# Optimization experiments

Measured on AMD Instinct MI355X. Metric: run time of the kernel, lower is better.

The kernel has to match this reference:

```python
import jax, jax.numpy as jnp
import numpy as np

B, S, D = 2, 2048, 2048
H = 32
HD = D // H  # 64
EPS = 1e-4


def setup_inputs() -> dict:
    key = jax.random.key(0)
    ks = jax.random.split(key, 9)
    hidden_states = jax.random.normal(ks[0], (B, S, D), dtype=jnp.float32)
    # multiplicative causal mask
    attention_mask = jnp.tril(jnp.ones((S, S), dtype=jnp.float32))[None, None]
    scale = 0.02
    wq = jax.random.normal(ks[1], (D, D), dtype=jnp.float32) * scale
    wk = jax.random.normal(ks[2], (D, D), dtype=jnp.float32) * scale
    wv = jax.random.normal(ks[3], (D, D), dtype=jnp.float32) * scale
    wo = jax.random.normal(ks[4], (D, D), dtype=jnp.float32) * scale
    bq = jax.random.normal(ks[5], (D,), dtype=jnp.float32) * scale
    bk = jax.random.normal(ks[6], (D,), dtype=jnp.float32) * scale
    bv = jax.random.normal(ks[7], (D,), dtype=jnp.float32) * scale
    bo = jax.random.normal(ks[8], (D,), dtype=jnp.float32) * scale
    return {"hidden_states": hidden_states, "attention_mask": attention_mask,
            "wq": wq, "bq": bq, "wk": wk, "bk": bk, "wv": wv, "bv": bv,
            "wo": wo, "bo": bo}


def _split_heads(x):
    # [B, S, D] -> [B, H, S, HD]
    b, s, _ = x.shape
    return x.reshape(b, s, H, HD).transpose(0, 2, 1, 3)


def reference(hidden_states, attention_mask, wq, bq, wk, bk, wv, bv, wo, bo):
    scaling = HD ** -0.5
    q = (hidden_states @ wq.T + bq) * scaling
    k = hidden_states @ wk.T + bk
    v = hidden_states @ wv.T + bv
    q, k, v = _split_heads(q), _split_heads(k), _split_heads(v)
    # ELU+1 feature map, then sum-normalize over head dim
    q = jax.nn.elu(q) + 1.0
    k = jax.nn.elu(k) + 1.0
    q = q / (q.sum(-1, keepdims=True) + EPS)
    k = k / (k.sum(-1, keepdims=True) + EPS)
    # quadratic attention: [B, H, S, S]
    attn = jnp.einsum('bhsd,bhtd->bhst', q, k) * (HD ** -0.5)
    attn = attn * attention_mask  # multiplicative mask
    out = jnp.einsum('bhst,bhtd->bhsd', attn, v)  # [B, H, S, HD]
    out = out.transpose(0, 2, 1, 3).reshape(hidden_states.shape[0], -1, D)
    return out @ wo.T + bo
```

## Files before the change

kernel.cpp:

```cpp
#include <hip/hip_runtime.h>

typedef __bf16 bf16x8 __attribute__((ext_vector_type(8)));
typedef float f32x4 __attribute__((ext_vector_type(4)));

#define GLDS(g, l) __builtin_amdgcn_global_load_lds(                              \
    (const __attribute__((address_space(1))) void*)(g),                            \
    (__attribute__((address_space(3))) void*)(l), 16, 0, 0)

__device__ __forceinline__ unsigned short f2bf(float f) {
  unsigned int u = __builtin_bit_cast(unsigned int, f);
  u = (u + 0x7fffu + ((u >> 16) & 1u)) >> 16;
  return (unsigned short)u;
}
__device__ __forceinline__ float bf2f(unsigned short h) {
  unsigned int u = ((unsigned int)h) << 16;
  return __builtin_bit_cast(float, u);
}

__global__ __launch_bounds__(256) void cvt_f32_bf16(
    const float* __restrict__ in, unsigned short* __restrict__ out, int n4) {
  int i = blockIdx.x * 256 + threadIdx.x;
  if (i < n4) {
    float4 v = ((const float4*)in)[i];
    ushort4 o;
    o.x = f2bf(v.x); o.y = f2bf(v.y); o.z = f2bf(v.z); o.w = f2bf(v.w);
    ((ushort4*)out)[i] = o;
  }
}

__global__ __launch_bounds__(256) void cvt_w4(
    const float* __restrict__ w0, const float* __restrict__ w1,
    const float* __restrict__ w2, const float* __restrict__ w3,
    unsigned short* __restrict__ out) {
  const int y = blockIdx.y;
  const float* src = (y == 0) ? w0 : (y == 1) ? w1 : (y == 2) ? w2 : w3;
  const int i = blockIdx.x * 256 + threadIdx.x;
  float4 v = ((const float4*)src)[i];
  ushort4 o;
  o.x = f2bf(v.x); o.y = f2bf(v.y); o.z = f2bf(v.z); o.w = f2bf(v.w);
  ((ushort4*)(out + (size_t)y * 4194304))[i] = o;
}

__global__ __launch_bounds__(512, 2) void gemm384_qkv(
    const unsigned short* __restrict__ A, const unsigned short* __restrict__ Bw,
    const float* __restrict__ bq, const float* __restrict__ bk, const float* __restrict__ bv,
    unsigned short* __restrict__ oQ, unsigned short* __restrict__ oK,
    unsigned short* __restrict__ oV) {
  constexpr int K = 2048, NT = 32;
  __shared__ unsigned short lds[81920];
  const int tid = threadIdx.x, lane = tid & 63, wid = tid >> 6;
  const int wm = wid >> 1, wn = wid & 1;

  const int g0 = blockIdx.x;
  const int wg = (g0 & 7) * 32 + (g0 >> 3);
  const int chunk = wg >> 5, l = wg & 31;
  const int bx = (chunk & 3) * 4 + (l >> 3);
  const int by = (chunk >> 2) * 8 + (l & 7);

  const int rloc = tid >> 3;
  const size_t gcoff = (size_t)(((lane & 7) ^ (lane >> 3)) << 3);
  const unsigned short* gA = A  + (size_t)(by * 256 + rloc) * K + gcoff;
  const unsigned short* gB = Bw + (size_t)(bx * 384 + rloc) * K + gcoff;

#define ABu(b) ((b) * 16384)
#define BBu(b) (32768 + (b) * 24576)
#define STAGE_A(c, b) GLDS(gA + (size_t)(c) * 64 * K, lds + ABu(b) + (c) * 4096 + wid * 512)
#define STAGE_B(c, b) GLDS(gB + (size_t)(c) * 64 * K, lds + BBu(b) + (c) * 4096 + wid * 512)

  const int arow = (wm * 64 + (lane & 15)) * 64;
  const int brow = (wn * 192 + (lane & 15)) * 64;
  const int sw0 = (((lane >> 4)) ^ (lane & 7)) << 3;
  const int sw1 = ((4 + (lane >> 4)) ^ (lane & 7)) << 3;

  f32x4 acc[4][12] = {};

  STAGE_A(0, 0); STAGE_A(1, 0); STAGE_A(2, 0); STAGE_A(3, 0);
  STAGE_B(0, 0); STAGE_B(1, 0); STAGE_B(2, 0); STAGE_B(3, 0); STAGE_B(4, 0); STAGE_B(5, 0);
  gA += 64; gB += 64;
  asm volatile("s_waitcnt vmcnt(0)" ::: "memory");
  __builtin_amdgcn_s_barrier();

  for (int t = 0; t < NT; ++t) {
    const int Ab = ABu(t & 1) + arow;
    const int Bb = BBu(t & 1) + brow;
    const int sb = (t + 1) & 1;
    const bool st = (t + 1 < NT);
    bf16x8 Af[4], Bf[6];

    if (st) { STAGE_B(0, sb); STAGE_B(1, sb); STAGE_B(2, sb); }
#pragma unroll
    for (int m = 0; m < 4; ++m) Af[m] = *(const bf16x8*)&lds[Ab + m * 1024 + sw0];
#pragma unroll
    for (int n = 0; n < 6; ++n) Bf[n] = *(const bf16x8*)&lds[Bb + n * 1024 + sw0];
    __builtin_amdgcn_s_barrier();
    __builtin_amdgcn_s_setprio(1);
#pragma unroll
    for (int m = 0; m < 4; ++m)
#pragma unroll
      for (int n = 0; n < 6; ++n)
        acc[m][n] = __builtin_amdgcn_mfma_f32_16x16x32_bf16(Af[m], Bf[n], acc[m][n], 0, 0, 0);
    __builtin_amdgcn_s_setprio(0);
    __builtin_amdgcn_s_barrier();

    if (st) { STAGE_B(3, sb); STAGE_B(4, sb); STAGE_B(5, sb); }
#pragma unroll
    for (int n = 0; n < 6; ++n) Bf[n] = *(const bf16x8*)&lds[Bb + (n + 6) * 1024 + sw0];
    __builtin_amdgcn_s_barrier();
    __builtin_amdgcn_s_setprio(1);
#pragma unroll
    for (int m = 0; m < 4; ++m)
#pragma unroll
      for (int n = 0; n < 6; ++n)
        acc[m][n + 6] = __builtin_amdgcn_mfma_f32_16x16x32_bf16(Af[m], Bf[n], acc[m][n + 6], 0, 0, 0);
    __builtin_amdgcn_s_setprio(0);
    __builtin_amdgcn_s_barrier();

    if (st) { STAGE_A(0, sb); STAGE_A(1, sb); STAGE_A(2, sb); STAGE_A(3, sb); }
#pragma unroll
    for (int m = 0; m < 4; ++m) Af[m] = *(const bf16x8*)&lds[Ab + m * 1024 + sw1];
#pragma unroll
    for (int n = 0; n < 6; ++n) Bf[n] = *(const bf16x8*)&lds[Bb + n * 1024 + sw1];
    __builtin_amdgcn_s_barrier();
    __builtin_amdgcn_s_setprio(1);
#pragma unroll
    for (int m = 0; m < 4; ++m)
#pragma unroll
      for (int n = 0; n < 6; ++n)
        acc[m][n] = __builtin_amdgcn_mfma_f32_16x16x32_bf16(Af[m], Bf[n], acc[m][n], 0, 0, 0);
    __builtin_amdgcn_s_setprio(0);
    __builtin_amdgcn_s_barrier();

#pragma unroll
    for (int n = 0; n < 6; ++n) Bf[n] = *(const bf16x8*)&lds[Bb + (n + 6) * 1024 + sw1];
    __builtin_amdgcn_s_barrier();
    __builtin_amdgcn_s_setprio(1);
#pragma unroll
    for (int m = 0; m < 4; ++m)
#pragma unroll
      for (int n = 0; n < 6; ++n)
        acc[m][n + 6] = __builtin_amdgcn_mfma_f32_16x16x32_bf16(Af[m], Bf[n], acc[m][n + 6], 0, 0, 0);
    __builtin_amdgcn_s_setprio(0);
    if (st) {
      gA += 64; gB += 64;
      asm volatile("s_waitcnt vmcnt(0)" ::: "memory");
    }
    __builtin_amdgcn_s_barrier();
  }

  const int head0 = bx * 6 + wn * 3;
#pragma unroll
  for (int g = 0; g < 3; ++g) {
    const int head = head0 + g;
    const int type = head >> 5;
    const int h = head & 31;
    const float* bias = (type == 0) ? bq : (type == 1) ? bk : bv;
    unsigned short* dst = (type == 0) ? oQ : (type == 1) ? oK : oV;
    float bv4[4];
#pragma unroll
    for (int j = 0; j < 4; ++j) bv4[j] = bias[h * 64 + j * 16 + (lane & 15)];
#pragma unroll
    for (int m = 0; m < 4; ++m) {
#pragma unroll
      for (int r = 0; r < 4; ++r) {
        const int row = by * 256 + wm * 64 + m * 16 + ((lane >> 4) << 2) + r;
        const int bb = row >> 11, s = row & 2047;
        float e[4];
        float loc = 0.f;
#pragma unroll
        for (int j = 0; j < 4; ++j) {
          float v = acc[m][g * 4 + j][r] + bv4[j];
          if (type == 0) v *= 0.125f;
          if (type < 2) v = (v > 0.f) ? (v + 1.f) : __expf(v);
          e[j] = v; loc += v;
        }
        if (type < 2) {
#pragma unroll
          for (int off = 1; off < 16; off <<= 1) loc += __shfl_xor(loc, off, 64);
          const float inv = 1.f / (loc + 1e-4f);
#pragma unroll
          for (int j = 0; j < 4; ++j) e[j] *= inv;
        }
        const size_t base = ((size_t)((bb << 5) + h) * 2048 + s) * 64;
#pragma unroll
        for (int j = 0; j < 4; ++j) dst[base + j * 16 + (lane & 15)] = f2bf(e[j]);
      }
    }
  }
#undef ABu
#undef BBu
#undef STAGE_A
#undef STAGE_B
}

__global__ __launch_bounds__(512, 2) void gemm128_wo(
    const unsigned short* __restrict__ A, const unsigned short* __restrict__ Bw,
    const float* __restrict__ b0, float* __restrict__ C) {
  constexpr int K = 2048, NT = 32;
  __shared__ unsigned short lds[73728];
  const int tid = threadIdx.x, lane = tid & 63, wid = tid >> 6;
  const int wm = wid >> 2, wn = wid & 3;

  const int g0 = blockIdx.x;
  const int wg = (g0 & 7) * 32 + (g0 >> 3);
  const int l = wg % 32;
  const int chunk = wg / 32;
  const int bx2 = (chunk % 4) * 2 + l / 16;
  const int by2 = (chunk / 4) * 16 + l % 16;

  const int rloc = wid * 8 + (lane >> 3);
  const size_t gcoff = (size_t)(((lane & 7) ^ (lane >> 3)) << 3);
  const unsigned short* gA[2];
  const unsigned short* gB[4];
#pragma unroll
  for (int c = 0; c < 2; ++c) gA[c] = A + (size_t)(by2 * 128 + c * 64 + rloc) * K + gcoff;
#pragma unroll
  for (int c = 0; c < 4; ++c) gB[c] = Bw + (size_t)(bx2 * 256 + c * 64 + rloc) * K + gcoff;

  int aoff[4][2], boff[4][2];
#pragma unroll
  for (int m = 0; m < 4; ++m)
#pragma unroll
    for (int kk = 0; kk < 2; ++kk) {
      aoff[m][kk] = (wm * 64 + m * 16 + (lane & 15)) * 64 +
                    ((((kk << 2) + (lane >> 4)) ^ (lane & 7)) << 3);
      boff[m][kk] = (wn * 64 + m * 16 + (lane & 15)) * 64 +
                    ((((kk << 2) + (lane >> 4)) ^ (lane & 7)) << 3);
    }

  f32x4 acc[4][4] = {};

#define AB(b) ((b) * 8192)
#define BB(b) (24576 + (b) * 16384)
#define STAGE_A(c, b) GLDS(gA[c], lds + AB(b) + (c) * 4096 + wid * 512)
#define STAGE_B(c, b) GLDS(gB[c], lds + BB(b) + (c) * 4096 + wid * 512)

  STAGE_A(0, 0); STAGE_A(1, 0); STAGE_B(0, 0); STAGE_B(1, 0); STAGE_B(2, 0); STAGE_B(3, 0);
#pragma unroll
  for (int c = 0; c < 2; ++c) gA[c] += 64;
#pragma unroll
  for (int c = 0; c < 4; ++c) gB[c] += 64;
  STAGE_A(0, 1); STAGE_A(1, 1); STAGE_B(0, 1); STAGE_B(1, 1); STAGE_B(2, 1); STAGE_B(3, 1);
#pragma unroll
  for (int c = 0; c < 2; ++c) gA[c] += 64;
#pragma unroll
  for (int c = 0; c < 4; ++c) gB[c] += 64;
  asm volatile("s_waitcnt vmcnt(6)" ::: "memory");
  __builtin_amdgcn_s_barrier();

  for (int t = 0; t < NT; ++t) {
    const int b = t % 3;
    const int sb = (t + 2) % 3;
    const bool doStage = (t + 2 < NT);

    if (doStage) { STAGE_A(0, sb); STAGE_A(1, sb); STAGE_B(0, sb); STAGE_B(1, sb); }
    bf16x8 af[4], bfr[4];
#pragma unroll
    for (int m = 0; m < 4; ++m) af[m] = *(const bf16x8*)&lds[AB(b) + aoff[m][0]];
#pragma unroll
    for (int n = 0; n < 4; ++n) bfr[n] = *(const bf16x8*)&lds[BB(b) + boff[n][0]];
    __builtin_amdgcn_s_barrier();
    __builtin_amdgcn_s_setprio(1);
#pragma unroll
    for (int m = 0; m < 4; ++m)
#pragma unroll
      for (int n = 0; n < 4; ++n)
        acc[m][n] = __builtin_amdgcn_mfma_f32_16x16x32_bf16(af[m], bfr[n], acc[m][n], 0, 0, 0);
    __builtin_amdgcn_s_setprio(0);
    __builtin_amdgcn_s_barrier();

    if (doStage) { STAGE_B(2, sb); STAGE_B(3, sb); }
#pragma unroll
    for (int c = 0; c < 2; ++c) gA[c] += 64;
#pragma unroll
    for (int c = 0; c < 4; ++c) gB[c] += 64;
#pragma unroll
    for (int m = 0; m < 4; ++m) af[m] = *(const bf16x8*)&lds[AB(b) + aoff[m][1]];
#pragma unroll
    for (int n = 0; n < 4; ++n) bfr[n] = *(const bf16x8*)&lds[BB(b) + boff[n][1]];
    __builtin_amdgcn_s_barrier();
    __builtin_amdgcn_s_setprio(1);
#pragma unroll
    for (int m = 0; m < 4; ++m)
#pragma unroll
      for (int n = 0; n < 4; ++n)
        acc[m][n] = __builtin_amdgcn_mfma_f32_16x16x32_bf16(af[m], bfr[n], acc[m][n], 0, 0, 0);
    __builtin_amdgcn_s_setprio(0);
    if (t < NT - 1) {
      if (doStage) asm volatile("s_waitcnt vmcnt(6)" ::: "memory");
      else         asm volatile("s_waitcnt vmcnt(0)" ::: "memory");
    }
    __builtin_amdgcn_s_barrier();
  }

#pragma unroll
  for (int n = 0; n < 4; ++n) {
    const int col = bx2 * 256 + wn * 64 + n * 16 + (lane & 15);
    const float bv_ = b0[col];
#pragma unroll
    for (int m = 0; m < 4; ++m) {
      const int row0 = by2 * 128 + wm * 64 + m * 16 + ((lane >> 4) << 2);
#pragma unroll
      for (int r = 0; r < 4; ++r)
        C[(size_t)(row0 + r) * 2048 + col] = acc[m][n][r] + bv_;
    }
  }
#undef AB
#undef BB
#undef STAGE_A
#undef STAGE_B
}

__global__ __launch_bounds__(256) void chunk_state(
    const unsigned short* __restrict__ Kn, const unsigned short* __restrict__ Vn,
    unsigned short* __restrict__ stT) {
  __shared__ unsigned short Kt[64 * 72];
  __shared__ unsigned short Vt[64 * 72];
  const int c = blockIdx.x, bh = blockIdx.y;
  const int tid = threadIdx.x, lane = tid & 63, wid = tid >> 6;
  const size_t base = (size_t)bh * 2048 * 64 + (size_t)c * 64 * 64;
#pragma unroll
  for (int i = 0; i < 16; ++i) {
    const int ii = i * 256 + tid;
    const int t = ii >> 6, d = ii & 63;
    Kt[d * 72 + t] = Kn[base + ii];
    Vt[d * 72 + t] = Vn[base + ii];
  }
  __syncthreads();
  f32x4 acc[4] = {};
#pragma unroll
  for (int ks = 0; ks < 2; ++ks) {
    const int ko = ks * 32 + (lane >> 4) * 8;
    bf16x8 a = *(const bf16x8*)&Vt[(wid * 16 + (lane & 15)) * 72 + ko];
#pragma unroll
    for (int ej = 0; ej < 4; ++ej) {
      bf16x8 bb = *(const bf16x8*)&Kt[(ej * 16 + (lane & 15)) * 72 + ko];
      acc[ej] = __builtin_amdgcn_mfma_f32_16x16x32_bf16(a, bb, acc[ej], 0, 0, 0);
    }
  }
  const size_t obase = ((size_t)bh * 32 + c) * 4096;
#pragma unroll
  for (int ej = 0; ej < 4; ++ej) {
    const int e = ej * 16 + (lane & 15);
    const int d0 = wid * 16 + ((lane >> 4) << 2);
#pragma unroll
    for (int r = 0; r < 4; ++r)
      stT[obase + (size_t)(d0 + r) * 64 + e] = f2bf(acc[ej][r]);
  }
}

__global__ __launch_bounds__(256) void prefix_state(
    const unsigned short* __restrict__ stT, unsigned short* __restrict__ cumT) {
  const int g = blockIdx.x * 256 + threadIdx.x;
  const int bh = g >> 12, e = g & 4095;
  float run = 0.f;
  for (int c = 0; c < 32; ++c) {
    const size_t idx = (((size_t)bh * 32 + c) << 12) + e;
    const float v = bf2f(stT[idx]);
    cumT[idx] = f2bf(run);
    run += v;
  }
}

__global__ __launch_bounds__(256) void attn_intra(
    const unsigned short* __restrict__ Qn, const unsigned short* __restrict__ Kn,
    const unsigned short* __restrict__ Vn, const unsigned short* __restrict__ cumT,
    unsigned short* __restrict__ aout) {
  __shared__ unsigned short Qs[64 * 72];
  __shared__ unsigned short Ks[64 * 72];
  __shared__ unsigned short Vt[64 * 72];
  __shared__ unsigned short St[64 * 72];
  __shared__ unsigned short Ps[64 * 72];
  const int c = blockIdx.x, bh = blockIdx.y;
  const int tid = threadIdx.x, lane = tid & 63, wid = tid >> 6;
  const size_t base = (size_t)bh * 2048 * 64 + (size_t)c * 64 * 64;
  const size_t sbase = ((size_t)bh * 32 + c) * 4096;
#pragma unroll
  for (int i = 0; i < 16; ++i) {
    const int ii = i * 256 + tid;
    const int t = ii >> 6, d = ii & 63;
    Qs[t * 72 + d] = Qn[base + ii];
    Ks[t * 72 + d] = Kn[base + ii];
    Vt[d * 72 + t] = Vn[base + ii];
    St[t * 72 + d] = cumT[sbase + ii];
  }
  __syncthreads();
  f32x4 sacc[4] = {};
#pragma unroll
  for (int ks = 0; ks < 2; ++ks) {
    const int ko = ks * 32 + (lane >> 4) * 8;
    bf16x8 a = *(const bf16x8*)&Qs[(wid * 16 + (lane & 15)) * 72 + ko];
#pragma unroll
    for (int tj = 0; tj < 4; ++tj) {
      bf16x8 bb = *(const bf16x8*)&Ks[(tj * 16 + (lane & 15)) * 72 + ko];
      sacc[tj] = __builtin_amdgcn_mfma_f32_16x16x32_bf16(a, bb, sacc[tj], 0, 0, 0);
    }
  }
#pragma unroll
  for (int tj = 0; tj < 4; ++tj) {
    const int t = tj * 16 + (lane & 15);
    const int s0 = wid * 16 + ((lane >> 4) << 2);
#pragma unroll
    for (int r = 0; r < 4; ++r) {
      const float v = (t <= s0 + r) ? sacc[tj][r] : 0.f;
      Ps[(s0 + r) * 72 + t] = f2bf(v);
    }
  }
  __syncthreads();
  f32x4 oacc[4] = {};
#pragma unroll
  for (int ks = 0; ks < 2; ++ks) {
    const int ko = ks * 32 + (lane >> 4) * 8;
    bf16x8 a = *(const bf16x8*)&Ps[(wid * 16 + (lane & 15)) * 72 + ko];
    bf16x8 a2 = *(const bf16x8*)&Qs[(wid * 16 + (lane & 15)) * 72 + ko];
#pragma unroll
    for (int dj = 0; dj < 4; ++dj) {
      bf16x8 bv_ = *(const bf16x8*)&Vt[(dj * 16 + (lane & 15)) * 72 + ko];
      oacc[dj] = __builtin_amdgcn_mfma_f32_16x16x32_bf16(a, bv_, oacc[dj], 0, 0, 0);
      bf16x8 bs_ = *(const bf16x8*)&St[(dj * 16 + (lane & 15)) * 72 + ko];
      oacc[dj] = __builtin_amdgcn_mfma_f32_16x16x32_bf16(a2, bs_, oacc[dj], 0, 0, 0);
    }
  }
  const int b = bh >> 5, h = bh & 31;
#pragma unroll
  for (int dj = 0; dj < 4; ++dj) {
    const int d = dj * 16 + (lane & 15);
    const int s0 = wid * 16 + ((lane >> 4) << 2);
#pragma unroll
    for (int r = 0; r < 4; ++r) {
      const size_t row = (size_t)(b * 2048 + c * 64 + s0 + r);
      aout[row * 2048 + h * 64 + d] = f2bf(0.125f * oacc[dj][r]);
    }
  }
}

extern "C" void kernel_launch(void* const* d_in, const int* in_sizes, int n_in,
                              void* d_out, int out_size, void* d_ws, size_t ws_size,
                              hipStream_t stream) {
  const float* hs = (const float*)d_in[0];
  const float* wq = (const float*)d_in[2];
  const float* bq = (const float*)d_in[3];
  const float* wk = (const float*)d_in[4];
  const float* bk = (const float*)d_in[5];
  const float* wv = (const float*)d_in[6];
  const float* bv = (const float*)d_in[7];
  const float* wo = (const float*)d_in[8];
  const float* bo = (const float*)d_in[9];
  float* out = (float*)d_out;
  char* ws = (char*)d_ws;

  unsigned short* hs_bf   = (unsigned short*)(ws);
  unsigned short* wall_bf = (unsigned short*)(ws + 16777216);
  unsigned short* Qn      = (unsigned short*)(ws + 50331648);
  unsigned short* Kn      = (unsigned short*)(ws + 67108864);
  unsigned short* Vn      = (unsigned short*)(ws + 83886080);
  unsigned short* stT     = (unsigned short*)(ws + 100663296);
  unsigned short* cumT    = (unsigned short*)(ws + 117440512);
  unsigned short* aout    = (unsigned short*)(ws + 134217728);

  cvt_f32_bf16<<<8192, 256, 0, stream>>>(hs, hs_bf, 2097152);
  cvt_w4<<<dim3(4096, 4), 256, 0, stream>>>(wq, wk, wv, wo, wall_bf);

  gemm384_qkv<<<256, 512, 0, stream>>>(hs_bf, wall_bf, bq, bk, bv, Qn, Kn, Vn);

  chunk_state<<<dim3(32, 64), 256, 0, stream>>>(Kn, Vn, stT);
  prefix_state<<<1024, 256, 0, stream>>>(stT, cumT);
  attn_intra<<<dim3(32, 64), 256, 0, stream>>>(Qn, Kn, Vn, cumT, aout);

  gemm128_wo<<<256, 512, 0, stream>>>(aout, wall_bf + 12582912, bo, out);
}
```

Measured before the change: 200.6 us.

## Split QKV GEMM K-tiles into half-slabs with deeper partial-vmcnt prefetch pipeline

Restructures the QKV GEMM's LDS staging so each 64-wide K tile is split into two 32-wide sub-slabs with their own buffers. Loads for the next half-tile and the tile after are issued early, and the full vmcnt(0) drain is replaced by partial vmcnt(10) waits, so global loads stay in flight across iterations. The swizzle and LDS addressing change to match the 32-element row layout. This adds complexity in the wait-count bookkeeping and risks bank conflicts with the new swizzle.

After: 211.9 us. 5.6% more time.

```diff
diff --git a/kernel.cpp b/kernel.cpp
--- a/kernel.cpp
+++ b/kernel.cpp
@@ -57,41 +57,44 @@
   const int bx = (chunk & 3) * 4 + (l >> 3);
   const int by = (chunk >> 2) * 8 + (l & 7);
 
-  const int rloc = tid >> 3;
-  const size_t gcoff = (size_t)(((lane & 7) ^ (lane >> 3)) << 3);
-  const unsigned short* gA = A  + (size_t)(by * 256 + rloc) * K + gcoff;
-  const unsigned short* gB = Bw + (size_t)(bx * 384 + rloc) * K + gcoff;
-
-#define ABu(b) ((b) * 16384)
-#define BBu(b) (32768 + (b) * 24576)
-#define STAGE_A(c, b) GLDS(gA + (size_t)(c) * 64 * K, lds + ABu(b) + (c) * 4096 + wid * 512)
-#define STAGE_B(c, b) GLDS(gB + (size_t)(c) * 64 * K, lds + BBu(b) + (c) * 4096 + wid * 512)
-
-  const int arow = (wm * 64 + (lane & 15)) * 64;
-  const int brow = (wn * 192 + (lane & 15)) * 64;
-  const int sw0 = (((lane >> 4)) ^ (lane & 7)) << 3;
-  const int sw1 = ((4 + (lane >> 4)) ^ (lane & 7)) << 3;
+  const int srow = tid >> 2;
+  const size_t gsw = (size_t)(((tid & 3) ^ (srow & 3)) << 3);
+  const unsigned short* gAb = A  + (size_t)(by * 256 + srow) * K + gsw;
+  const unsigned short* gBb = Bw + (size_t)(bx * 384 + srow) * K + gsw;
+
+#define STAGE_SUB(tt, h)                                                                      \
+  do {                                                                                        \
+    const int _sl = 2 * ((tt) & 1) + (h);                                                     \
+    const size_t _go = (size_t)(tt) * 64 + (h) * 32;                                          \
+    GLDS(gAb + _go,           lds + _sl * 8192 + wid * 512);                                  \
+    GLDS(gAb + _go + 128 * K, lds + _sl * 8192 + 4096 + wid * 512);                           \
+    GLDS(gBb + _go,           lds + 32768 + _sl * 12288 + wid * 512);                         \
+    GLDS(gBb + _go + 128 * K, lds + 32768 + _sl * 12288 + 4096 + wid * 512);                  \
+    GLDS(gBb + _go + 256 * K, lds + 32768 + _sl * 12288 + 8192 + wid * 512);                  \
+  } while (0)
+
+  const int rchk = ((lane >> 4) ^ (lane & 3)) << 3;
+  const int arow = (wm * 64 + (lane & 15)) * 32 + rchk;
+  const int brow = (wn * 192 + (lane & 15)) * 32 + rchk;
 
   f32x4 acc[4][12] = {};
 
-  STAGE_A(0, 0); STAGE_A(1, 0); STAGE_A(2, 0); STAGE_A(3, 0);
-  STAGE_B(0, 0); STAGE_B(1, 0); STAGE_B(2, 0); STAGE_B(3, 0); STAGE_B(4, 0); STAGE_B(5, 0);
-  gA += 64; gB += 64;
-  asm volatile("s_waitcnt vmcnt(0)" ::: "memory");
+  STAGE_SUB(0, 0); STAGE_SUB(0, 1); STAGE_SUB(1, 0);
+  asm volatile("s_waitcnt vmcnt(10)" ::: "memory");
   __builtin_amdgcn_s_barrier();
 
   for (int t = 0; t < NT; ++t) {
-    const int Ab = ABu(t & 1) + arow;
-    const int Bb = BBu(t & 1) + brow;
-    const int sb = (t + 1) & 1;
-    const bool st = (t + 1 < NT);
+    const int a0 = (2 * (t & 1)) * 8192 + arow;
+    const int b0 = 32768 + (2 * (t & 1)) * 12288 + brow;
+    const int a1 = a0 + 8192;
+    const int b1 = b0 + 12288;
     bf16x8 Af[4], Bf[6];
 
-    if (st) { STAGE_B(0, sb); STAGE_B(1, sb); STAGE_B(2, sb); }
-#pragma unroll
-    for (int m = 0; m < 4; ++m) Af[m] = *(const bf16x8*)&lds[Ab + m * 1024 + sw0];
-#pragma unroll
-    for (int n = 0; n < 6; ++n) Bf[n] = *(const bf16x8*)&lds[Bb + n * 1024 + sw0];
+    if (t + 1 < NT) STAGE_SUB(t + 1, 1);
+#pragma unroll
+    for (int m = 0; m < 4; ++m) Af[m] = *(const bf16x8*)&lds[a0 + m * 512];
+#pragma unroll
+    for (int n = 0; n < 6; ++n) Bf[n] = *(const bf16x8*)&lds[b0 + n * 512];
     __builtin_amdgcn_s_barrier();
     __builtin_amdgcn_s_setprio(1);
 #pragma unroll
@@ -102,9 +105,8 @@
     __builtin_amdgcn_s_setprio(0);
     __builtin_amdgcn_s_barrier();
 
-    if (st) { STAGE_B(3, sb); STAGE_B(4, sb); STAGE_B(5, sb); }
-#pragma unroll
-    for (int n = 0; n < 6; ++n) Bf[n] = *(const bf16x8*)&lds[Bb + (n + 6) * 1024 + sw0];
+#pragma unroll
+    for (int n = 0; n < 6; ++n) Bf[n] = *(const bf16x8*)&lds[b0 + (n + 6) * 512];
     __builtin_amdgcn_s_barrier();
     __builtin_amdgcn_s_setprio(1);
 #pragma unroll
@@ -113,13 +115,15 @@
       for (int n = 0; n < 6; ++n)
         acc[m][n + 6] = __builtin_amdgcn_mfma_f32_16x16x32_bf16(Af[m], Bf[n], acc[m][n + 6], 0, 0, 0);
     __builtin_amdgcn_s_setprio(0);
-    __builtin_amdgcn_s_barrier();
-
-    if (st) { STAGE_A(0, sb); STAGE_A(1, sb); STAGE_A(2, sb); STAGE_A(3, sb); }
-#pragma unroll
-    for (int m = 0; m < 4; ++m) Af[m] = *(const bf16x8*)&lds[Ab + m * 1024 + sw1];
-#pragma unroll
-    for (int n = 0; n < 6; ++n) Bf[n] = *(const bf16x8*)&lds[Bb + n * 1024 + sw1];
+    if (t < NT - 1) asm volatile("s_waitcnt vmcnt(10)" ::: "memory");
+    else            asm volatile("s_waitcnt vmcnt(0)" ::: "memory");
+    __builtin_amdgcn_s_barrier();
+
+    if (t + 2 < NT) STAGE_SUB(t + 2, 0);
+#pragma unroll
+    for (int m = 0; m < 4; ++m) Af[m] = *(const bf16x8*)&lds[a1 + m * 512];
+#pragma unroll
+    for (int n = 0; n < 6; ++n) Bf[n] = *(const bf16x8*)&lds[b1 + n * 512];
     __builtin_amdgcn_s_barrier();
     __builtin_amdgcn_s_setprio(1);
 #pragma unroll
@@ -131,7 +135,7 @@
     __builtin_amdgcn_s_barrier();
 
 #pragma unroll
-    for (int n = 0; n < 6; ++n) Bf[n] = *(const bf16x8*)&lds[Bb + (n + 6) * 1024 + sw1];
+    for (int n = 0; n < 6; ++n) Bf[n] = *(const bf16x8*)&lds[b1 + (n + 6) * 512];
     __builtin_amdgcn_s_barrier();
     __builtin_amdgcn_s_setprio(1);
 #pragma unroll
@@ -140,10 +144,8 @@
       for (int n = 0; n < 6; ++n)
         acc[m][n + 6] = __builtin_amdgcn_mfma_f32_16x16x32_bf16(Af[m], Bf[n], acc[m][n + 6], 0, 0, 0);
     __builtin_amdgcn_s_setprio(0);
-    if (st) {
-      gA += 64; gB += 64;
-      asm volatile("s_waitcnt vmcnt(0)" ::: "memory");
-    }
+    if (t < NT - 2)      asm volatile("s_waitcnt vmcnt(10)" ::: "memory");
+    else if (t == NT - 2) asm volatile("s_waitcnt vmcnt(5)" ::: "memory");
     __builtin_amdgcn_s_barrier();
   }
 
@@ -186,10 +188,7 @@
       }
     }
   }
-#undef ABu
-#undef BBu
-#undef STAGE_A
-#undef STAGE_B
+#undef STAGE_SUB
 }
 
 __global__ __launch_bounds__(512, 2) void gemm128_wo(
```
